# Kernel optimization log

Hardware: AMD Instinct MI355X
Metric: run time of the kernel (lower is better)

Reference implementation:

```python
import jax, jax.numpy as jnp
import numpy as np

D_MODEL = 512
D_ALPHA = 100
D_PH = 80
SCALE = 1.0 / np.sqrt(D_MODEL)


def gru_cell(x, h, Wih, Whh, bih, bhh):
    # PyTorch GRU gate order: r, z, n
    gi = x @ Wih.T + bih
    gh = h @ Whh.T + bhh
    ir, iz, inn = jnp.split(gi, 3, axis=-1)
    hr, hz, hn = jnp.split(gh, 3, axis=-1)
    r = jax.nn.sigmoid(ir + hr)
    z = jax.nn.sigmoid(iz + hz)
    n = jnp.tanh(inn + r * hn)
    return (1.0 - z) * n + z * h


def attend(q, k, v):
    # q: [B,D], k/v: [B,L,D]
    scores = jnp.einsum('bd,bld->bl', q, k) * SCALE
    a = jax.nn.softmax(scores, axis=-1)  # [B,L]
    o = jnp.einsum('bl,bld->bd', a, v)
    return a, o


def setup_inputs() -> dict:
    key = jax.random.key(0)
    ks = jax.random.split(key, 25)
    D = D_MODEL

    def u(k, shape, fan):
        return jax.random.uniform(k, shape, jnp.float32, -1.0, 1.0) / np.sqrt(fan)

    inp = {
        'text': jax.random.randint(ks[0], (256, 128), 0, D_ALPHA),
        'tgt': jax.random.randint(ks[1], (256, 64), 0, D_PH),
        'E_alpha': jax.random.normal(ks[2], (D_ALPHA, D), jnp.float32),
        'enc_Wih_f': u(ks[3], (3 * D, D), D),
        'enc_Whh_f': u(ks[4], (3 * D, D), D),
        'enc_bih_f': u(ks[5], (3 * D,), D),
        'enc_bhh_f': u(ks[6], (3 * D,), D),
        'enc_Wih_b': u(ks[7], (3 * D, D), D),
        'enc_Whh_b': u(ks[8], (3 * D, D), D),
        'enc_bih_b': u(ks[9], (3 * D,), D),
        'enc_bhh_b': u(ks[10], (3 * D,), D),
        'hpost_W': u(ks[11], (D, 2 * D), 2 * D),
        'hpost_b': u(ks[12], (D,), 2 * D),
        'wk_W': u(ks[13], (D, 2 * D), 2 * D),
        'wk_b': u(ks[14], (D,), 2 * D),
        'wv_W': u(ks[15], (D, 2 * D), 2 * D),
        'wv_b': u(ks[16], (D,), 2 * D),
        'E_ph': jax.random.normal(ks[17], (D_PH, D), jnp.float32),
        'dec_Wih': u(ks[18], (3 * D, 2 * D), 2 * D),
        'dec_Whh': u(ks[19], (3 * D, D), D),
        'dec_bih': u(ks[20], (3 * D,), D),
        'dec_bhh': u(ks[21], (3 * D,), D),
        'post_W': u(ks[22], (D_PH, D), D),
        'post_b': u(ks[23], (D_PH,), D),
    }
    return inp


def reference(text, tgt, E_alpha, enc_Wih_f, enc_Whh_f, enc_bih_f, enc_bhh_f,
              enc_Wih_b, enc_Whh_b, enc_bih_b, enc_bhh_b, hpost_W, hpost_b,
              wk_W, wk_b, wv_W, wv_b, E_ph, dec_Wih, dec_Whh, dec_bih,
              dec_bhh, post_W, post_b):
    B, LT = text.shape
    LP = tgt.shape[1]

    # ---- Encoder: bidirectional single-layer GRU (eval: dropout = identity)
    emb = E_alpha[text]                     # [B,LT,D]
    xs = jnp.swapaxes(emb, 0, 1)            # [LT,B,D]
    h0 = jnp.zeros((B, D_MODEL), emb.dtype)

    def mk_step(Wih, Whh, bih, bhh):
        def step(h, x):
            h2 = gru_cell(x, h, Wih, Whh, bih, bhh)
            return h2, h2
        return step

    hF, ysF = jax.lax.scan(mk_step(enc_Wih_f, enc_Whh_f, enc_bih_f, enc_bhh_f), h0, xs)
    hB, ysB = jax.lax.scan(mk_step(enc_Wih_b, enc_Whh_b, enc_bih_b, enc_bhh_b), h0, xs[::-1])
    ysB = ysB[::-1]
    enc_o = jnp.swapaxes(jnp.concatenate([ysF, ysB], axis=-1), 0, 1)  # [B,LT,2D]
    h = jnp.tanh(jnp.concatenate([hF, hB], axis=-1) @ hpost_W.T + hpost_b)  # [B,D]

    k = enc_o @ wk_W.T + wk_b               # [B,LT,D]
    v = enc_o @ wv_W.T + wv_b               # [B,LT,D]

    # ---- initial attention from encoder hidden; eval-mode first token is argmax
    # over tgt[:,0] reshaped to [B,1,1], i.e. always index 0.
    a_sl0, a_o0 = attend(h, k, v)
    dec_i0 = jnp.zeros((B,), jnp.int32)

    def dstep(carry, _):
        hh, a_o, a_sl, dec_i = carry
        e = E_ph[dec_i]                                  # [B,D]
        x = gru_cell(jnp.concatenate([e, a_o], axis=-1), hh,
                     dec_Wih, dec_Whh, dec_bih, dec_bhh)  # [B,D]
        o = x @ post_W.T + post_b                         # [B,D_PH]
        n_sl, n_o = attend(x, k, v)
        nxt = jnp.argmax(o, axis=-1).astype(jnp.int32)
        return (x, n_o, n_sl, nxt), (a_sl, o)

    _, (attn_t, res_t) = jax.lax.scan(dstep, (h, a_o0, a_sl0, dec_i0), None, length=LP)
    attn = jnp.swapaxes(attn_t, 0, 1)        # [B,LP,LT]
    res = jnp.swapaxes(res_t, 0, 1)          # [B,LP,D_PH]
    return attn, res
```

## Files before the change

### kernel.cpp

```cpp
#include <hip/hip_runtime.h>
#include <math.h>

#define B   256
#define LT  128
#define LP  64
#define DM  512
#define D3  1536
#define DPH 80
#define SCALE_F 0.044194173824159216f

__device__ __forceinline__ float dot4(float4 a, float4 b) {
    return a.x*b.x + a.y*b.y + a.z*b.z + a.w*b.w;
}
__device__ __forceinline__ float sigmoidf_(float x) {
    return 1.0f / (1.0f + expf(-x));
}

__device__ __forceinline__ float4 issue_bypass4(const float* p) {
    float4 v;
    asm volatile("global_load_dwordx4 %0, %1, off sc0 sc1"
                 : "=v"(v) : "v"(p));
    return v;
}
__device__ __forceinline__ void wait_vm0() {
    asm volatile("s_waitcnt vmcnt(0)" ::: "memory");
    __builtin_amdgcn_sched_barrier(0);
}

__device__ __forceinline__ void group_barrier(int* cnt, int target) {
    __syncthreads();
    if (threadIdx.x == 0) {
        __hip_atomic_fetch_add(cnt, 1, __ATOMIC_RELEASE,
                               __HIP_MEMORY_SCOPE_AGENT);
        while (__hip_atomic_load(cnt, __ATOMIC_RELAXED,
                                 __HIP_MEMORY_SCOPE_AGENT) < target)
            __builtin_amdgcn_s_sleep(16);
    }
    __syncthreads();
}

__global__ __launch_bounds__(256) void precompG_kernel(
    const float* __restrict__ Emb, const float* __restrict__ W,
    const float* __restrict__ bias, float* __restrict__ G,
    int wstride, int woff)
{
    const int n  = blockIdx.x * 256 + threadIdx.x;
    const int r0 = blockIdx.y * 4;
    __shared__ float es[4][DM];
    for (int i = threadIdx.x; i < 4 * DM; i += 256)
        es[i >> 9][i & 511] = Emb[(r0 + (i >> 9)) * DM + (i & 511)];
    __syncthreads();
    float acc[4] = {0.f, 0.f, 0.f, 0.f};
    const float* wr = &W[(size_t)n * wstride + woff];
    for (int j = 0; j < DM; j += 4) {
        float4 w4 = *(const float4*)&wr[j];
        #pragma unroll
        for (int rr = 0; rr < 4; ++rr) {
            float4 e4 = *(const float4*)&es[rr][j];
            acc[rr] += dot4(e4, w4);
        }
    }
    float bv = bias[n];
    #pragma unroll
    for (int rr = 0; rr < 4; ++rr)
        G[(r0 + rr) * D3 + n] = acc[rr] + bv;
}

__global__ __launch_bounds__(512, 1) void enc_persist_kernel(
    const float* __restrict__ Gf, const float* __restrict__ Gb,
    const float* __restrict__ Whh_f, const float* __restrict__ Whh_b,
    const float* __restrict__ bhh_f, const float* __restrict__ bhh_b,
    const int* __restrict__ text,
    float* __restrict__ hF0, float* __restrict__ hF1,
    float* __restrict__ hB0, float* __restrict__ hB1,
    float* __restrict__ E,
    const float* __restrict__ hpost_W, const float* __restrict__ hpost_b,
    float* __restrict__ hd0, int* __restrict__ bar)
{
    __shared__ float Wl[48][516];
    __shared__ float As[2][64][36];
    __shared__ float xs[1024];
    __shared__ float bl[48];

    const int tid  = threadIdx.x;
    const int blk  = blockIdx.x;
    const int dir  = blk & 1;
    const int bblk = (blk >> 1) & 3;
    const int jblk = blk >> 3;
    const int jtile = jblk * 16;
    const int btile = bblk * 64;
    int* cnt = bar + (blk & 7);

    const float* G   = dir ? Gb : Gf;
    const float* Whh = dir ? Whh_b : Whh_f;
    const float* bhh = dir ? bhh_b : bhh_f;
    float* h0 = dir ? hB0 : hF0;
    float* h1 = dir ? hB1 : hF1;
    const int yoff = dir ? DM : 0;

    for (int i = tid; i < 48 * 128; i += 512) {
        const int r = i >> 7, c = (i & 127) << 2;
        *(float4*)&Wl[r][c] =
            *(const float4*)&Whh[(size_t)((r >> 4) * DM + jtile + (r & 15)) * DM + c];
    }
    if (tid < 48) bl[tid] = bhh[(tid >> 4) * DM + jtile + (tid & 15)];
    __syncthreads();

    const int jj   = tid & 15;
    const int rg   = tid >> 4;
    const int lrow = tid >> 3;
    const int lcol = (tid & 7) * 4;

    for (int s = 0; s < LT; ++s) {
        const int t = dir ? (LT - 1 - s) : s;
        const float* hin = (s & 1) ? h1 : h0;
        float* hout      = (s & 1) ? h0 : h1;

        float acc[2][3];
        #pragma unroll
        for (int m = 0; m < 2; ++m) {
            acc[m][0] = 0.f; acc[m][1] = 0.f; acc[m][2] = 0.f;
        }

        float4 rA = issue_bypass4(&hin[(btile + lrow) * DM + lcol]);
        wait_vm0();
        int buf = 0;
        for (int kc = 0; kc < 16; ++kc) {
            *(float4*)&As[buf][lrow][lcol] = rA;
            __syncthreads();
            float4 nA;
            if (kc < 15)
                nA = issue_bypass4(&hin[(btile + lrow) * DM + (kc + 1) * 32 + lcol]);
            const int kb = kc * 32;
            #pragma unroll
            for (int c4 = 0; c4 < 8; ++c4) {
                float4 bv0 = *(float4*)&Wl[jj][kb + c4 * 4];
                float4 bv1 = *(float4*)&Wl[16 + jj][kb + c4 * 4];
                float4 bv2 = *(float4*)&Wl[32 + jj][kb + c4 * 4];
                #pragma unroll
                for (int m = 0; m < 2; ++m) {
                    float4 av = *(float4*)&As[buf][rg * 2 + m][c4 * 4];
                    acc[m][0] += dot4(av, bv0);
                    acc[m][1] += dot4(av, bv1);
                    acc[m][2] += dot4(av, bv2);
                }
            }
            if (kc < 15) { wait_vm0(); rA = nA; }
            buf ^= 1;
        }

        const int j = jtile + jj;
        #pragma unroll
        for (int m = 0; m < 2; ++m) {
            const int b = btile + rg * 2 + m;
            const int c = text[b * LT + t];
            float hr = acc[m][0] + bl[jj];
            float hz = acc[m][1] + bl[16 + jj];
            float hn = acc[m][2] + bl[32 + jj];
            float r = sigmoidf_(G[c * D3 + j] + hr);
            float z = sigmoidf_(G[c * D3 + DM + j] + hz);
            float n = tanhf(G[c * D3 + 2 * DM + j] + r * hn);
            float hp = hin[b * DM + j];
            float hv = (1.f - z) * n + z * hp;
            hout[b * DM + j] = hv;
            E[(size_t)(b * LT + t) * 1024 + yoff + j] = hv;
        }
        if (s < LT - 1) group_barrier(cnt, 32 * (s + 1));
    }

    group_barrier(bar + 8, 256);
    {
        const int b = blk;
        if (tid < 256) {
            float4 v = issue_bypass4((tid < 128)
                ? &hF0[b * DM + tid * 4]
                : &hB0[b * DM + (tid - 128) * 4]);
            wait_vm0();
            *(float4*)&xs[tid * 4] = v;
        }
        __syncthreads();
        if (tid < DM) {
            const float* wr = &hpost_W[tid * 1024];
            float acc = 0.f;
            for (int jx = 0; jx < 1024; jx += 4)
                acc += dot4(*(const float4*)&xs[jx], *(const float4*)&wr[jx]);
            hd0[b * DM + tid] = tanhf(acc + hpost_b[tid]);
        }
    }
}

__global__ __launch_bounds__(256) void kv_chunk_kernel(
    const float* __restrict__ E,
    const float* __restrict__ wk, const float* __restrict__ wv,
    const float* __restrict__ kb, const float* __restrict__ vb,
    float* __restrict__ T, int r0)
{
    __shared__ float As[64][36];
    __shared__ float Bk[64][36];
    __shared__ float Bv[64][36];
    const int tid = threadIdx.x;
    const int nn = tid & 15, bb = tid >> 4;
    const int ntile = blockIdx.x * 64;
    const int mtile = blockIdx.y * 64;

    float ak[4][4], av_[4][4];
    #pragma unroll
    for (int m = 0; m < 4; ++m)
        #pragma unroll
        for (int i = 0; i < 4; ++i) { ak[m][i] = 0.f; av_[m][i] = 0.f; }

    const int lrow = tid >> 3;
    const int lcol = (tid & 7) * 4;

    for (int k0 = 0; k0 < 1024; k0 += 32) {
        __syncthreads();
        *(float4*)&As[lrow][lcol] =
            *(const float4*)&E[(size_t)(r0 + mtile + lrow) * 1024 + k0 + lcol];
        *(float4*)&As[lrow + 32][lcol] =
            *(const float4*)&E[(size_t)(r0 + mtile + lrow + 32) * 1024 + k0 + lcol];
        *(float4*)&Bk[lrow][lcol] =
            *(const float4*)&wk[(ntile + lrow) * 1024 + k0 + lcol];
        *(float4*)&Bk[lrow + 32][lcol] =
            *(const float4*)&wk[(ntile + lrow + 32) * 1024 + k0 + lcol];
        *(float4*)&Bv[lrow][lcol] =
            *(const float4*)&wv[(ntile + lrow) * 1024 + k0 + lcol];
        *(float4*)&Bv[lrow + 32][lcol] =
            *(const float4*)&wv[(ntile + lrow + 32) * 1024 + k0 + lcol];
        __syncthreads();
        #pragma unroll
        for (int c4 = 0; c4 < 8; ++c4) {
            float4 a4[4], k4[4], v4[4];
            #pragma unroll
            for (int m = 0; m < 4; ++m) a4[m] = *(float4*)&As[bb + 16 * m][c4 * 4];
            #pragma unroll
            for (int i = 0; i < 4; ++i) {
                k4[i] = *(float4*)&Bk[nn + 16 * i][c4 * 4];
                v4[i] = *(float4*)&Bv[nn + 16 * i][c4 * 4];
            }
            #pragma unroll
            for (int m = 0; m < 4; ++m)
                #pragma unroll
                for (int i = 0; i < 4; ++i) {
                    ak[m][i]  += dot4(a4[m], k4[i]);
                    av_[m][i] += dot4(a4[m], v4[i]);
                }
        }
    }
    #pragma unroll
    for (int m = 0; m < 4; ++m) {
        const int lm = mtile + bb + 16 * m;
        #pragma unroll
        for (int i = 0; i < 4; ++i) {
            const int gn = ntile + nn + 16 * i;
            T[(size_t)lm * 1024 + gn]       = ak[m][i]  + kb[gn];
            T[(size_t)lm * 1024 + DM + gn]  = av_[m][i] + vb[gn];
        }
    }
}

__global__ __launch_bounds__(256) void copy4_kernel(
    float4* __restrict__ dst, const float4* __restrict__ src, int n4)
{
    int i = blockIdx.x * 256 + threadIdx.x;
    const int stride = gridDim.x * 256;
    for (; i < n4; i += stride) dst[i] = src[i];
}

__device__ __forceinline__ void attend_body(
    int b, int tid, const float* __restrict__ q, const float* __restrict__ EKV,
    const float* __restrict__ post_W, const float* __restrict__ post_b,
    float* __restrict__ attn, float* __restrict__ res,
    float* __restrict__ a_o, int* __restrict__ dec_i,
    int s, int attn_row, int do_post, int do_attn,
    float* qs, float* part, float* sarr, float* red, float4 (*pvp)[128])
{
    if (tid < 128) {
        float4 qv = issue_bypass4(&q[b * DM + tid * 4]);
        wait_vm0();
        *(float4*)&qs[tid * 4] = qv;
    }
    __syncthreads();

    if (do_post) {
        if (tid < DPH) {
            const float* wr = &post_W[tid * DM];
            float acc = 0.f;
            for (int d = 0; d < DM; d += 4)
                acc += dot4(*(const float4*)&qs[d], *(const float4*)&wr[d]);
            float lv = acc + post_b[tid];
            res[(size_t)(b * LP + s) * DPH + tid] = lv;
            part[tid] = lv;
        }
        __syncthreads();
        if (tid == 0) {
            float best = part[0]; int bi = 0;
            for (int p = 1; p < DPH; ++p) {
                float vv = part[p];
                if (vv > best) { best = vv; bi = p; }
            }
            dec_i[b] = bi;
        }
        __syncthreads();
    }

    if (do_attn) {
        {
            const int r = tid & 127, quad = tid >> 7;
            const float* kr = &EKV[(size_t)(b * LT + r) * 1024 + quad * 128];
            const float* qh = &qs[quad * 128];
            float p0 = 0.f, p1 = 0.f;
            #pragma unroll
            for (int d = 0; d < 128; d += 8) {
                p0 += dot4(*(const float4*)&qh[d],     *(const float4*)&kr[d]);
                p1 += dot4(*(const float4*)&qh[d + 4], *(const float4*)&kr[d + 4]);
            }
            part[tid] = p0 + p1;
        }
        __syncthreads();
        if (tid < LT)
            sarr[tid] = (((part[tid] + part[tid + 128]) + part[tid + 256])
                         + part[tid + 384]) * SCALE_F;
        __syncthreads();
        if (tid < 64) {
            float m = fmaxf(sarr[tid], sarr[tid + 64]);
            #pragma unroll
            for (int off = 32; off > 0; off >>= 1)
                m = fmaxf(m, __shfl_xor(m, off));
            if (tid == 0) red[0] = m;
        }
        __syncthreads();
        const float smax = red[0];
        if (tid < LT) sarr[tid] = expf(sarr[tid] - smax);
        __syncthreads();
        if (tid < 64) {
            float ssum = sarr[tid] + sarr[tid + 64];
            #pragma unroll
            for (int off = 32; off > 0; off >>= 1)
                ssum += __shfl_xor(ssum, off);
            if (tid == 0) red[1] = ssum;
        }
        __syncthreads();
        const float inv = 1.0f / red[1];
        if (tid < LT) {
            float a = sarr[tid] * inv;
            sarr[tid] = a;
            attn[(size_t)(b * LP + attn_row) * LT + tid] = a;
        }
        __syncthreads();
        {
            const int d4 = tid & 127, quad = tid >> 7;
            const float* vb0 = &EKV[(size_t)b * LT * 1024 + DM];
            float4 a0 = make_float4(0.f, 0.f, 0.f, 0.f);
            float4 a1 = make_float4(0.f, 0.f, 0.f, 0.f);
            const int l0 = quad * 32;
            #pragma unroll
            for (int l = l0; l < l0 + 32; l += 2) {
                float w0 = sarr[l], w1 = sarr[l + 1];
                float4 v0 = *(const float4*)&vb0[(size_t)l * 1024 + d4 * 4];
                float4 v1 = *(const float4*)&vb0[(size_t)(l + 1) * 1024 + d4 * 4];
                a0.x += w0 * v0.x; a0.y += w0 * v0.y;
                a0.z += w0 * v0.z; a0.w += w0 * v0.w;
                a1.x += w1 * v1.x; a1.y += w1 * v1.y;
                a1.z += w1 * v1.z; a1.w += w1 * v1.w;
            }
            pvp[quad][d4] = make_float4(a0.x + a1.x, a0.y + a1.y,
                                        a0.z + a1.z, a0.w + a1.w);
        }
        __syncthreads();
        if (tid < 128) {
            float4 p0 = pvp[0][tid], p1 = pvp[1][tid];
            float4 p2 = pvp[2][tid], p3 = pvp[3][tid];
            float4 o = make_float4(((p0.x + p1.x) + p2.x) + p3.x,
                                   ((p0.y + p1.y) + p2.y) + p3.y,
                                   ((p0.z + p1.z) + p2.z) + p3.z,
                                   ((p0.w + p1.w) + p2.w) + p3.w);
            *(float4*)&a_o[b * DM + tid * 4] = o;
        }
    }
}

__global__ __launch_bounds__(512, 1) void dec_persist_kernel(
    const float* __restrict__ Gd,
    const float* __restrict__ dec_Wih, const float* __restrict__ dec_Whh,
    const float* __restrict__ dec_bhh,
    const float* __restrict__ EKV,
    const float* __restrict__ post_W, const float* __restrict__ post_b,
    float* __restrict__ attn, float* __restrict__ res,
    float* __restrict__ a_o, int* __restrict__ dec_i,
    float* __restrict__ hd0, float* __restrict__ hd1,
    int* __restrict__ bar)
{
    __shared__ float Wi[24][516];
    __shared__ float Wh[24][516];
    __shared__ float As[2][64][36];
    __shared__ float bl[24];
    __shared__ float qs[DM];
    __shared__ float part[512];
    __shared__ float sarr[LT];
    __shared__ float red[2];
    __shared__ float4 pvp[4][128];

    const int tid  = threadIdx.x;
    const int blk  = blockIdx.x;
    const int bblk = blk & 3;
    const int jblk = blk >> 2;
    const int jtile = jblk * 8;
    const int btile = bblk * 64;
    const int arow  = btile + jblk;
    int* cnt = bar + 9 + bblk;
    int nb = 0;

    for (int i = tid; i < 24 * 128; i += 512) {
        const int r = i >> 7, c = (i & 127) << 2;
        const int wrow = (r >> 3) * DM + jtile + (r & 7);
        *(float4*)&Wi[r][c] =
            *(const float4*)&dec_Wih[(size_t)wrow * 1024 + DM + c];
        *(float4*)&Wh[r][c] =
            *(const float4*)&dec_Whh[(size_t)wrow * DM + c];
    }
    if (tid < 24) bl[tid] = dec_bhh[(tid >> 3) * DM + jtile + (tid & 7)];
    __syncthreads();

    attend_body(arow, tid, hd0, EKV, post_W, post_b, attn, res, a_o, dec_i,
                0, 0, 0, 1, qs, part, sarr, red, pvp);
    ++nb; group_barrier(cnt, 64 * nb);

    const int jj   = tid & 7;
    const int rr   = tid >> 3;
    const int lrow = tid >> 3;
    const int lcol = (tid & 7) * 4;

    for (int s = 0; s < LP; ++s) {
        const float* hin = (s & 1) ? hd1 : hd0;
        float* hout      = (s & 1) ? hd0 : hd1;

        float acc[4] = {0.f, 0.f, 0.f, 0.f};

        #pragma unroll
        for (int ph = 0; ph < 2; ++ph) {
            const float* Aptr = (ph == 0) ? a_o : hin;
            const float (*W)[516] = (ph == 0) ? Wi : Wh;

            float4 rA = issue_bypass4(&Aptr[(btile + lrow) * DM + lcol]);
            wait_vm0();
            int buf = (ph == 0) ? 0 : 0;
            for (int kc = 0; kc < 16; ++kc) {
                *(float4*)&As[buf][lrow][lcol] = rA;
                __syncthreads();
                float4 nA;
                if (kc < 15)
                    nA = issue_bypass4(&Aptr[(btile + lrow) * DM + (kc + 1) * 32 + lcol]);
                const int kb = kc * 32;
                #pragma unroll
                for (int c4 = 0; c4 < 8; ++c4) {
                    float4 bv0 = *(float4*)&W[jj][kb + c4 * 4];
                    float4 bv1 = *(float4*)&W[8 + jj][kb + c4 * 4];
                    float4 bv2 = *(float4*)&W[16 + jj][kb + c4 * 4];
                    float4 av  = *(float4*)&As[buf][rr][c4 * 4];
                    acc[0]      += dot4(av, bv0);
                    acc[1]      += dot4(av, bv1);
                    acc[2 + ph] += dot4(av, bv2);
                }
                if (kc < 15) { wait_vm0(); rA = nA; }
                buf ^= 1;
            }
            __syncthreads();
        }

        {
            const int j = jtile + jj;
            const int b = btile + rr;
            const int c = __hip_atomic_load(&dec_i[b], __ATOMIC_RELAXED,
                                            __HIP_MEMORY_SCOPE_SYSTEM);
            float r = sigmoidf_(Gd[c * D3 + j] + bl[jj] + acc[0]);
            float z = sigmoidf_(Gd[c * D3 + DM + j] + bl[8 + jj] + acc[1]);
            float n = tanhf(Gd[c * D3 + 2 * DM + j] + acc[2]
                            + r * (acc[3] + bl[16 + jj]));
            float hp = hin[b * DM + j];
            hout[b * DM + j] = (1.f - z) * n + z * hp;
        }
        ++nb; group_barrier(cnt, 64 * nb);

        attend_body(arow, tid, hout, EKV, post_W, post_b, attn, res, a_o, dec_i,
                    s, s + 1, 1, (s < LP - 1) ? 1 : 0,
                    qs, part, sarr, red, pvp);
        if (s < LP - 1) { ++nb; group_barrier(cnt, 64 * nb); }
    }
}

extern "C" void kernel_launch(void* const* d_in, const int* in_sizes, int n_in,
                              void* d_out, int out_size, void* d_ws, size_t ws_size,
                              hipStream_t stream)
{
    const int*   text    = (const int*)d_in[0];
    const float* E_alpha = (const float*)d_in[2];
    const float* Wih_f   = (const float*)d_in[3];
    const float* Whh_f   = (const float*)d_in[4];
    const float* bih_f   = (const float*)d_in[5];
    const float* bhh_f   = (const float*)d_in[6];
    const float* Wih_b   = (const float*)d_in[7];
    const float* Whh_b   = (const float*)d_in[8];
    const float* bih_b   = (const float*)d_in[9];
    const float* bhh_b   = (const float*)d_in[10];
    const float* hpost_W = (const float*)d_in[11];
    const float* hpost_b = (const float*)d_in[12];
    const float* wk_W    = (const float*)d_in[13];
    const float* wk_b    = (const float*)d_in[14];
    const float* wv_W    = (const float*)d_in[15];
    const float* wv_b    = (const float*)d_in[16];
    const float* E_ph    = (const float*)d_in[17];
    const float* dec_Wih = (const float*)d_in[18];
    const float* dec_Whh = (const float*)d_in[19];
    const float* dec_bih = (const float*)d_in[20];
    const float* dec_bhh = (const float*)d_in[21];
    const float* post_W  = (const float*)d_in[22];
    const float* post_b  = (const float*)d_in[23];

    float* ws = (float*)d_ws;
    float* Gf  = ws;
    float* Gb  = Gf  + 153600;
    float* Gd  = Gb  + 153600;
    float* hF0 = Gd  + 122880;
    float* hF1 = hF0 + 131072;
    float* hB0 = hF1 + 131072;
    float* hB1 = hB0 + 131072;
    float* hd0 = hB1 + 131072;
    float* hd1 = hd0 + 131072;
    float* a_o = hd1 + 131072;
    int*   dec_i = (int*)(a_o + 131072);
    int*   bar   = dec_i + 256;
    float* E   = a_o + 131072 + 512;
    float* T   = E + 33554432;

    hipMemsetAsync(hF0, 0, 131072 * sizeof(float), stream);
    hipMemsetAsync(hB0, 0, 131072 * sizeof(float), stream);
    hipMemsetAsync(dec_i, 0, (256 + 16) * sizeof(int), stream);

    precompG_kernel<<<dim3(6, 25), 256, 0, stream>>>(E_alpha, Wih_f, bih_f, Gf, DM, 0);
    precompG_kernel<<<dim3(6, 25), 256, 0, stream>>>(E_alpha, Wih_b, bih_b, Gb, DM, 0);
    precompG_kernel<<<dim3(6, 20), 256, 0, stream>>>(E_ph, dec_Wih, dec_bih, Gd, 1024, 0);

    enc_persist_kernel<<<dim3(256), 512, 0, stream>>>(
        Gf, Gb, Whh_f, Whh_b, bhh_f, bhh_b, text,
        hF0, hF1, hB0, hB1, E, hpost_W, hpost_b, hd0, bar);

    for (int c = 0; c < 2; ++c) {
        const int r0 = c * 16384;
        kv_chunk_kernel<<<dim3(8, 256), 256, 0, stream>>>(
            E, wk_W, wv_W, wk_b, wv_b, T, r0);
        copy4_kernel<<<dim3(4096), 256, 0, stream>>>(
            (float4*)(E + (size_t)r0 * 1024), (const float4*)T,
            16384 * 1024 / 4);
    }

    float* attn = (float*)d_out;
    float* res  = attn + (size_t)B * LP * LT;

    dec_persist_kernel<<<dim3(256), 512, 0, stream>>>(
        Gd, dec_Wih, dec_Whh, dec_bhh, E, post_W, post_b,
        attn, res, a_o, dec_i, hd0, hd1, bar);
}
```

Baseline: 12.03 ms.

## Prefetch gate inputs before matmul, restructure attention loads, shorten barrier sleep

Loads of the precomputed input-gate values and the previous hidden state are moved ahead of the recurrent matmul in both the encoder and decoder loops, so their latency overlaps the compute instead of sitting after it. The attention score pass now gives each wave 16 key rows with a cross-lane shuffle reduction and double-buffered register loads. The value-weighted sum is also batched with register double-buffering. The spin-barrier sleep interval is shortened to cut wake-up latency. The trade-off is higher register pressure and more polling traffic on the atomic counter.

```diff
diff --git a/kernel.cpp b/kernel.cpp
--- a/kernel.cpp
+++ b/kernel.cpp
@@ -34,7 +34,7 @@
                                __HIP_MEMORY_SCOPE_AGENT);
         while (__hip_atomic_load(cnt, __ATOMIC_RELAXED,
                                  __HIP_MEMORY_SCOPE_AGENT) < target)
-            __builtin_amdgcn_s_sleep(16);
+            __builtin_amdgcn_s_sleep(2);
     }
     __syncthreads();
 }
@@ -110,11 +110,23 @@
     const int rg   = tid >> 4;
     const int lrow = tid >> 3;
     const int lcol = (tid & 7) * 4;
+    const int j    = jtile + jj;
 
     for (int s = 0; s < LT; ++s) {
         const int t = dir ? (LT - 1 - s) : s;
         const float* hin = (s & 1) ? h1 : h0;
         float* hout      = (s & 1) ? h0 : h1;
+
+        float pg[2][3], php[2];
+        #pragma unroll
+        for (int m = 0; m < 2; ++m) {
+            const int b = btile + rg * 2 + m;
+            const int c = text[b * LT + t];
+            pg[m][0] = G[c * D3 + j];
+            pg[m][1] = G[c * D3 + DM + j];
+            pg[m][2] = G[c * D3 + 2 * DM + j];
+            php[m]   = hin[b * DM + j];
+        }
 
         float acc[2][3];
         #pragma unroll
@@ -149,19 +161,16 @@
             buf ^= 1;
         }
 
-        const int j = jtile + jj;
         #pragma unroll
         for (int m = 0; m < 2; ++m) {
             const int b = btile + rg * 2 + m;
-            const int c = text[b * LT + t];
             float hr = acc[m][0] + bl[jj];
             float hz = acc[m][1] + bl[16 + jj];
             float hn = acc[m][2] + bl[32 + jj];
-            float r = sigmoidf_(G[c * D3 + j] + hr);
-            float z = sigmoidf_(G[c * D3 + DM + j] + hz);
-            float n = tanhf(G[c * D3 + 2 * DM + j] + r * hn);
-            float hp = hin[b * DM + j];
-            float hv = (1.f - z) * n + z * hp;
+            float r = sigmoidf_(pg[m][0] + hr);
+            float z = sigmoidf_(pg[m][1] + hz);
+            float n = tanhf(pg[m][2] + r * hn);
+            float hv = (1.f - z) * n + z * php[m];
             hout[b * DM + j] = hv;
             E[(size_t)(b * LT + t) * 1024 + yoff + j] = hv;
         }
@@ -305,21 +314,45 @@
 
     if (do_attn) {
         {
-            const int r = tid & 127, quad = tid >> 7;
-            const float* kr = &EKV[(size_t)(b * LT + r) * 1024 + quad * 128];
-            const float* qh = &qs[quad * 128];
-            float p0 = 0.f, p1 = 0.f;
-            #pragma unroll
-            for (int d = 0; d < 128; d += 8) {
-                p0 += dot4(*(const float4*)&qh[d],     *(const float4*)&kr[d]);
-                p1 += dot4(*(const float4*)&qh[d + 4], *(const float4*)&kr[d + 4]);
+            const int wave = tid >> 6, lane = tid & 63;
+            const float* kbase =
+                &EKV[((size_t)(b * LT + wave * 16)) * 1024 + lane * 8];
+            const float4 qa = *(const float4*)&qs[lane * 8];
+            const float4 qb = *(const float4*)&qs[lane * 8 + 4];
+            float4 c0[4][2], c1[4][2];
+            #pragma unroll
+            for (int i = 0; i < 4; ++i) {
+                c0[i][0] = *(const float4*)(kbase + (size_t)i * 1024);
+                c0[i][1] = *(const float4*)(kbase + (size_t)i * 1024 + 4);
             }
-            part[tid] = p0 + p1;
-        }
-        __syncthreads();
-        if (tid < LT)
-            sarr[tid] = (((part[tid] + part[tid + 128]) + part[tid + 256])
-                         + part[tid + 384]) * SCALE_F;
+            #pragma unroll
+            for (int ch = 0; ch < 4; ++ch) {
+                if (ch < 3) {
+                    #pragma unroll
+                    for (int i = 0; i < 4; ++i) {
+                        c1[i][0] = *(const float4*)
+                            (kbase + (size_t)((ch + 1) * 4 + i) * 1024);
+                        c1[i][1] = *(const float4*)
+                            (kbase + (size_t)((ch + 1) * 4 + i) * 1024 + 4);
+                    }
+                }
+                #pragma unroll
+                for (int i = 0; i < 4; ++i) {
+                    float p0 = dot4(qa, c0[i][0]);
+                    float p1 = dot4(qb, c0[i][1]);
+                    float p = p0 + p1;
+                    #pragma unroll
+                    for (int off = 1; off < 64; off <<= 1)
+                        p += __shfl_xor(p, off);
+                    if (lane == 0)
+                        sarr[wave * 16 + ch * 4 + i] = p * SCALE_F;
+                }
+                #pragma unroll
+                for (int i = 0; i < 4; ++i) {
+                    c0[i][0] = c1[i][0]; c0[i][1] = c1[i][1];
+                }
+            }
+        }
         __syncthreads();
         if (tid < 64) {
             float m = fmaxf(sarr[tid], sarr[tid + 64]);
@@ -349,19 +382,33 @@
         __syncthreads();
         {
             const int d4 = tid & 127, quad = tid >> 7;
-            const float* vb0 = &EKV[(size_t)b * LT * 1024 + DM];
+            const float* vb0 = &EKV[(size_t)b * LT * 1024 + DM + d4 * 4];
             float4 a0 = make_float4(0.f, 0.f, 0.f, 0.f);
             float4 a1 = make_float4(0.f, 0.f, 0.f, 0.f);
             const int l0 = quad * 32;
-            #pragma unroll
-            for (int l = l0; l < l0 + 32; l += 2) {
-                float w0 = sarr[l], w1 = sarr[l + 1];
-                float4 v0 = *(const float4*)&vb0[(size_t)l * 1024 + d4 * 4];
-                float4 v1 = *(const float4*)&vb0[(size_t)(l + 1) * 1024 + d4 * 4];
-                a0.x += w0 * v0.x; a0.y += w0 * v0.y;
-                a0.z += w0 * v0.z; a0.w += w0 * v0.w;
-                a1.x += w1 * v1.x; a1.y += w1 * v1.y;
-                a1.z += w1 * v1.z; a1.w += w1 * v1.w;
+            float4 v0[8], v1[8];
+            #pragma unroll
+            for (int k = 0; k < 8; ++k)
+                v0[k] = *(const float4*)(vb0 + (size_t)(l0 + k) * 1024);
+            #pragma unroll
+            for (int bat = 0; bat < 4; ++bat) {
+                if (bat < 3) {
+                    #pragma unroll
+                    for (int k = 0; k < 8; ++k)
+                        v1[k] = *(const float4*)
+                            (vb0 + (size_t)(l0 + (bat + 1) * 8 + k) * 1024);
+                }
+                const int lb = l0 + bat * 8;
+                #pragma unroll
+                for (int k = 0; k < 8; k += 2) {
+                    float w0 = sarr[lb + k], w1 = sarr[lb + k + 1];
+                    a0.x += w0 * v0[k].x;     a0.y += w0 * v0[k].y;
+                    a0.z += w0 * v0[k].z;     a0.w += w0 * v0[k].w;
+                    a1.x += w1 * v0[k + 1].x; a1.y += w1 * v0[k + 1].y;
+                    a1.z += w1 * v0[k + 1].z; a1.w += w1 * v0[k + 1].w;
+                }
+                #pragma unroll
+                for (int k = 0; k < 8; ++k) v0[k] = v1[k];
             }
             pvp[quad][d4] = make_float4(a0.x + a1.x, a0.y + a1.y,
                                         a0.z + a1.z, a0.w + a1.w);
@@ -429,11 +476,20 @@
     const int rr   = tid >> 3;
     const int lrow = tid >> 3;
     const int lcol = (tid & 7) * 4;
+    const int j    = jtile + jj;
+    const int b_   = btile + rr;
 
     for (int s = 0; s < LP; ++s) {
         const float* hin = (s & 1) ? hd1 : hd0;
         float* hout      = (s & 1) ? hd0 : hd1;
 
+        const int c_ = __hip_atomic_load(&dec_i[b_], __ATOMIC_RELAXED,
+                                         __HIP_MEMORY_SCOPE_SYSTEM);
+        const float pg0 = Gd[c_ * D3 + j];
+        const float pg1 = Gd[c_ * D3 + DM + j];
+        const float pg2 = Gd[c_ * D3 + 2 * DM + j];
+        const float php_ = hin[b_ * DM + j];
+
         float acc[4] = {0.f, 0.f, 0.f, 0.f};
 
         #pragma unroll
@@ -443,7 +499,7 @@
 
             float4 rA = issue_bypass4(&Aptr[(btile + lrow) * DM + lcol]);
             wait_vm0();
-            int buf = (ph == 0) ? 0 : 0;
+            int buf = 0;
             for (int kc = 0; kc < 16; ++kc) {
                 *(float4*)&As[buf][lrow][lcol] = rA;
                 __syncthreads();
@@ -468,16 +524,10 @@
         }
 
         {
-            const int j = jtile + jj;
-            const int b = btile + rr;
-            const int c = __hip_atomic_load(&dec_i[b], __ATOMIC_RELAXED,
-                                            __HIP_MEMORY_SCOPE_SYSTEM);
-            float r = sigmoidf_(Gd[c * D3 + j] + bl[jj] + acc[0]);
-            float z = sigmoidf_(Gd[c * D3 + DM + j] + bl[8 + jj] + acc[1]);
-            float n = tanhf(Gd[c * D3 + 2 * DM + j] + acc[2]
-                            + r * (acc[3] + bl[16 + jj]));
-            float hp = hin[b * DM + j];
-            hout[b * DM + j] = (1.f - z) * n + z * hp;
+            float r = sigmoidf_(pg0 + bl[jj] + acc[0]);
+            float z = sigmoidf_(pg1 + bl[8 + jj] + acc[1]);
+            float n = tanhf(pg2 + acc[2] + r * (acc[3] + bl[16 + jj]));
+            hout[b_ * DM + j] = (1.f - z) * n + z * php_;
         }
         ++nb; group_barrier(cnt, 64 * nb);
 
```

Measured after the change: 12.30 ms. +2.2%, slower.
